# Performance work log

Measured on AMD Instinct MI355X. Metric: run time of the kernel, lower is better.

## Reference

```python
import jax, jax.numpy as jnp
import numpy as np

H = 2304; I_FF = 9216; NH = 8; NKV = 4; HD = 256; W = 4096; V = 65536
EPS = 1e-6; SOFTCAP = 30.0; HALF = HD // 2; POS = W // 2  # current decode position
WSCALE = 0.02


def rmsnorm(x, w, eps=EPS):
    return x * jax.lax.rsqrt(jnp.mean(x * x, axis=-1, keepdims=True) + eps) * w


def setup_inputs() -> dict:
    key = jax.random.key(0)
    ks = jax.random.split(key, 16)
    # RoPE angles for position POS
    inv_freq = 1.0 / (10000.0 ** (jnp.arange(HALF, dtype=jnp.float32) / HALF))
    ang = POS * inv_freq
    # attention mask: allow slots <= POS, block the rest
    slot = jnp.arange(W)
    mask = jnp.where(slot <= POS, 0.0, -1e9).astype(jnp.float32).reshape(1, 1, 1, W)
    # one-hot scatter selector for the cache write
    update_idx = jnp.zeros((1, 1, W, 1), jnp.float32).at[0, 0, POS, 0].set(1.0)
    return {
        "hidden_prev": jax.random.normal(ks[0], (1, 1, H), jnp.float32),
        "embed_token": jax.random.normal(ks[1], (1, 1, H), jnp.float32),
        "kv_k_in": jax.random.normal(ks[2], (1, NKV, W, HD), jnp.float32),
        "kv_v_in": jax.random.normal(ks[3], (1, NKV, W, HD), jnp.float32),
        "cos": jnp.cos(ang),
        "sin": jnp.sin(ang),
        "mask": mask,
        "update_idx": update_idx,
        "in_h_w": jax.random.normal(ks[4], (H, H), jnp.float32) * WSCALE,
        "in_e_w": jax.random.normal(ks[5], (H, H), jnp.float32) * WSCALE,
        "input_ln_w": jnp.ones((H,), jnp.float32),
        "post_attn_ln_w": jnp.ones((H,), jnp.float32),
        "pre_ffn_ln_w": jnp.ones((H,), jnp.float32),
        "post_ffn_ln_w": jnp.ones((H,), jnp.float32),
        "final_ln_w": jnp.ones((H,), jnp.float32),
        "q_w": jax.random.normal(ks[6], (NH * HD, H), jnp.float32) * WSCALE,
        "k_w": jax.random.normal(ks[7], (NKV * HD, H), jnp.float32) * WSCALE,
        "v_w": jax.random.normal(ks[8], (NKV * HD, H), jnp.float32) * WSCALE,
        "o_w": jax.random.normal(ks[9], (H, NH * HD), jnp.float32) * WSCALE,
        "q_norm_w": jnp.ones((HD,), jnp.float32),
        "k_norm_w": jnp.ones((HD,), jnp.float32),
        "gate_w": jax.random.normal(ks[10], (I_FF, H), jnp.float32) * WSCALE,
        "up_w": jax.random.normal(ks[11], (I_FF, H), jnp.float32) * WSCALE,
        "down_w": jax.random.normal(ks[12], (H, I_FF), jnp.float32) * WSCALE,
        "lm_head_w": jax.random.normal(ks[13], (V, H), jnp.float32) * WSCALE,
    }


def reference(hidden_prev, embed_token, kv_k_in, kv_v_in, cos, sin, mask, update_idx,
              in_h_w, in_e_w, input_ln_w, post_attn_ln_w, pre_ffn_ln_w, post_ffn_ln_w,
              final_ln_w, q_w, k_w, v_w, o_w, q_norm_w, k_norm_w, gate_w, up_w, down_w,
              lm_head_w):
    # dual input projection (1x1 convs == linear)
    x = hidden_prev @ in_h_w.T + embed_token @ in_e_w.T          # [1,1,H]
    residual = x
    hn = rmsnorm(x, input_ln_w)
    # QKV
    q = (hn @ q_w.T).reshape(1, NH, 1, HD)
    k = (hn @ k_w.T).reshape(1, NKV, 1, HD)
    v = (hn @ v_w.T).reshape(1, NKV, 1, HD)
    q = rmsnorm(q, q_norm_w)
    k = rmsnorm(k, k_norm_w)
    # RoPE (half-split rotation)
    cos_r = cos.reshape(1, 1, 1, HALF)
    sin_r = sin.reshape(1, 1, 1, HALF)
    q1, q2 = q[..., :HALF], q[..., HALF:]
    q = jnp.concatenate([q1 * cos_r - q2 * sin_r, q2 * cos_r + q1 * sin_r], axis=-1)
    k1, k2 = k[..., :HALF], k[..., HALF:]
    k_rot = jnp.concatenate([k1 * cos_r - k2 * sin_r, k2 * cos_r + k1 * sin_r], axis=-1)
    # multiply-based KV cache update
    keep = 1.0 - update_idx                                      # [1,1,W,1]
    kv_k_out = kv_k_in * keep + k_rot * update_idx               # [1,NKV,W,HD]
    kv_v_out = kv_v_in * keep + v * update_idx
    # GQA expansion
    n_rep = NH // NKV
    k_exp = jnp.repeat(kv_k_out, n_rep, axis=1)                  # [1,NH,W,HD]
    v_exp = jnp.repeat(kv_v_out, n_rep, axis=1)
    # fp32 attention
    scale = 1.0 / np.sqrt(HD)
    attn = jnp.einsum('bhqd,bhkd->bhqk', q, k_exp) * scale + mask
    p = jax.nn.softmax(attn, axis=-1)
    out = jnp.einsum('bhqk,bhkd->bhqd', p, v_exp).reshape(1, 1, NH * HD)
    h_attn = rmsnorm(out @ o_w.T, post_attn_ln_w)
    x = residual + h_attn
    residual = x
    # FFN (gelu-gated)
    hf = rmsnorm(x, pre_ffn_ln_w)
    d = (jax.nn.gelu(hf @ gate_w.T, approximate=False) * (hf @ up_w.T)) @ down_w.T
    x = residual + rmsnorm(d, post_ffn_ln_w)
    hidden_out = rmsnorm(x, final_ln_w)
    # lm_head + softcap + argmax
    logits = hidden_out @ lm_head_w.T                            # [1,1,V]
    logits = jnp.tanh(logits / SOFTCAP) * SOFTCAP
    idx = jnp.argmax(logits, axis=-1)                            # [1,1]
    top_k_indices = idx.reshape(1).astype(jnp.int32)
    top_k_values = jnp.take_along_axis(logits, idx[..., None], axis=-1).reshape(1)
    return (top_k_indices, top_k_values, hidden_out, kv_k_out, kv_v_out)
```

## Files before the change

### kernel.cpp

```cpp
#include <hip/hip_runtime.h>
#include <math.h>

#define H      2304
#define I_FF   9216
#define NH     8
#define NKV    4
#define HD     256
#define W_CTX  4096
#define V_SZ   65536
#define POS    2048
#define NCHUNK 32
#define CHUNK  64
#define NATTN  (NH * NCHUNK)
#define NBLK_ATTN_TOTAL 2048
#define EPS    1e-6f
#define NBLK_IN   576
#define NBLK_LM   4096

enum {
  WS_X    = 0,
  WS_SSQ  = 2304,
  WS_QKV  = 2880,
  WS_ML   = 6976,
  WS_YP   = 7488,
  WS_HRAW = 73024,
  WS_X2   = 75328,
  WS_ACT  = 77632,
  WS_DV   = 86848,
  WS_PART = 89152,
  WS_END  = 97344
};

typedef float f4v __attribute__((ext_vector_type(4)));
typedef float f2v __attribute__((ext_vector_type(2)));

__device__ __forceinline__ f4v ntload4(const float* p) {
  return __builtin_nontemporal_load((const f4v*)p);
}
__device__ __forceinline__ float wave_reduce_sum(float v) {
#pragma unroll
  for (int off = 32; off; off >>= 1) v += __shfl_down(v, off);
  return v;
}
__device__ __forceinline__ float wave_reduce_max(float v) {
#pragma unroll
  for (int off = 32; off; off >>= 1) v = fmaxf(v, __shfl_down(v, off));
  return v;
}
__device__ __forceinline__ float dot4(float4 a, float4 b) {
  return a.x * b.x + a.y * b.y + a.z * b.z + a.w * b.w;
}
__device__ __forceinline__ float dot4n(f4v a, float4 b) {
  return a.x * b.x + a.y * b.y + a.z * b.z + a.w * b.w;
}

__global__ void k_input(const float* __restrict__ Wh, const float* __restrict__ We,
                        const float* __restrict__ hprev, const float* __restrict__ emb,
                        float* __restrict__ x, float* __restrict__ ssq_part) {
  __shared__ float sv[4];
  int wv = threadIdx.x >> 6, lane = threadIdx.x & 63;
  int row = blockIdx.x * 4 + wv;
  const float* wh = Wh + (size_t)row * H;
  const float* we = We + (size_t)row * H;
  const float4* hp = (const float4*)hprev;
  const float4* em = (const float4*)emb;
  float acc = 0.f;
#pragma unroll
  for (int i = 0; i < H / 256; ++i) {
    int idx = lane + i * 64;
    acc += dot4n(ntload4(wh + idx * 4), hp[idx]);
    acc += dot4n(ntload4(we + idx * 4), em[idx]);
  }
  acc = wave_reduce_sum(acc);
  if (lane == 0) { x[row] = acc; sv[wv] = acc * acc; }
  __syncthreads();
  if (threadIdx.x == 0) ssq_part[blockIdx.x] = sv[0] + sv[1] + sv[2] + sv[3];
}

__global__ void k_qkv(const float* __restrict__ qw, const float* __restrict__ kw,
                      const float* __restrict__ vw, const float* __restrict__ x,
                      const float* __restrict__ lnw, const float* __restrict__ ssq,
                      float* __restrict__ qkv) {
  __shared__ float sred[4];
  int tid = threadIdx.x, lane = tid & 63, wv = tid >> 6;
  float s = ssq[tid] + ssq[tid + 256] + (tid < 64 ? ssq[tid + 512] : 0.f);
  s = wave_reduce_sum(s);
  if (lane == 0) sred[wv] = s;
  __syncthreads();
  float scale = rsqrtf((sred[0] + sred[1] + sred[2] + sred[3]) / (float)H + EPS);

  int row = (blockIdx.x * 256 + tid) >> 6;
  const float* Wrow;
  if (row < 2048)      Wrow = qw + (size_t)row * H;
  else if (row < 3072) Wrow = kw + (size_t)(row - 2048) * H;
  else                 Wrow = vw + (size_t)(row - 3072) * H;
  const float4* xv = (const float4*)x;
  const float4* l4 = (const float4*)lnw;
  float acc = 0.f;
#pragma unroll
  for (int i = 0; i < H / 256; ++i) {
    int idx = lane + i * 64;
    f4v w = ntload4(Wrow + idx * 4);
    float4 hx = xv[idx], wl = l4[idx];
    acc += w.x * (hx.x * scale * wl.x) + w.y * (hx.y * scale * wl.y) +
           w.z * (hx.z * scale * wl.z) + w.w * (hx.w * scale * wl.w);
  }
  acc = wave_reduce_sum(acc);
  if (lane == 0) qkv[row] = acc;
}

__global__ void k_attn(const float* __restrict__ qkv, const float* __restrict__ qnw,
                       const float* __restrict__ knw, const float* __restrict__ cosv,
                       const float* __restrict__ sinv, const float* __restrict__ kin,
                       const float* __restrict__ vin, float* __restrict__ kv_k_out,
                       float* __restrict__ kv_v_out, float* __restrict__ ml,
                       float* __restrict__ ypart,
                       const f2v* __restrict__ kin2, const f2v* __restrict__ vin2,
                       f2v* __restrict__ kout2, f2v* __restrict__ vout2) {
  int b = blockIdx.x;
  int tid = threadIdx.x, lane = tid & 63, wv = tid >> 6;
  if (b >= NATTN) {
    size_t cb = b - NATTN;
    const size_t n = (size_t)NKV * W_CTX * HD / 2;
    const size_t stride = (size_t)(NBLK_ATTN_TOTAL - NATTN) * 256;
    for (size_t i = cb * 256 + tid; i < n; i += stride) {
      int slot = (int)((i >> 7) & (W_CTX - 1));
      if (slot != POS) {
        __builtin_nontemporal_store(kin2[i], kout2 + i);
        __builtin_nontemporal_store(vin2[i], vout2 + i);
      }
    }
    return;
  }
  int h = b >> 5, j = b & 31, kvh = h >> 1;
  __shared__ float qs[HD], ks[HD], sc[CHUNK + 1];
  __shared__ float sredq[4], sredk[4];
  float qv = qkv[h * HD + tid];
  float kv = qkv[2048 + kvh * HD + tid];
  float pq = wave_reduce_sum(qv * qv);
  float pk = wave_reduce_sum(kv * kv);
  if (lane == 0) { sredq[wv] = pq; sredk[wv] = pk; }
  __syncthreads();
  float sq = rsqrtf((sredq[0] + sredq[1] + sredq[2] + sredq[3]) / (float)HD + EPS);
  float sk = rsqrtf((sredk[0] + sredk[1] + sredk[2] + sredk[3]) / (float)HD + EPS);
  qs[tid] = qv * sq * qnw[tid];
  ks[tid] = kv * sk * knw[tid];
  __syncthreads();
  if (tid < HD / 2) {
    float c = cosv[tid], s2 = sinv[tid];
    float q1 = qs[tid], q2 = qs[tid + 128];
    qs[tid] = q1 * c - q2 * s2;  qs[tid + 128] = q2 * c + q1 * s2;
    float k1 = ks[tid], k2 = ks[tid + 128];
    ks[tid] = k1 * c - k2 * s2;  ks[tid + 128] = k2 * c + k1 * s2;
  }
  __syncthreads();
  if (j == 0 && (h & 1) == 0) {
    kv_k_out[((size_t)kvh * W_CTX + POS) * HD + tid] = ks[tid];
    kv_v_out[((size_t)kvh * W_CTX + POS) * HD + tid] = qkv[3072 + kvh * HD + tid];
  }
  int base = j * CHUNK;
  int clen = (j == NCHUNK - 1) ? CHUNK + 1 : CHUNK;
  float4 qf = ((const float4*)qs)[lane];
  const float4* Kb = (const float4*)(kin + ((size_t)kvh * W_CTX + base) * HD);
  for (int i = wv; i < clen; i += 4) {
    float4 kk = (i < CHUNK) ? Kb[(size_t)i * (HD / 4) + lane] : ((const float4*)ks)[lane];
    float acc = dot4(qf, kk);
    acc = wave_reduce_sum(acc);
    if (lane == 0) sc[i] = acc * 0.0625f;
  }
  __syncthreads();
  float m = -1e30f;
  for (int i = tid; i < clen; i += 256) m = fmaxf(m, sc[i]);
  m = wave_reduce_max(m);
  if (lane == 0) sredq[wv] = m;
  __syncthreads();
  float M = fmaxf(fmaxf(sredq[0], sredq[1]), fmaxf(sredq[2], sredq[3]));
  float ssum = 0.f;
  for (int i = tid; i < clen; i += 256) { float e = expf(sc[i] - M); sc[i] = e; ssum += e; }
  ssum = wave_reduce_sum(ssum);
  if (lane == 0) sredk[wv] = ssum;
  __syncthreads();
  if (tid == 0) {
    ml[(h * NCHUNK + j) * 2]     = M;
    ml[(h * NCHUNK + j) * 2 + 1] = sredk[0] + sredk[1] + sredk[2] + sredk[3];
  }
  const float* Vb = vin + ((size_t)kvh * W_CTX + base) * HD;
  float a0 = 0.f, a1 = 0.f, a2 = 0.f, a3 = 0.f;
  for (int s = 0; s < CHUNK; s += 4) {
    a0 += sc[s]     * Vb[(size_t)s * HD + tid];
    a1 += sc[s + 1] * Vb[(size_t)(s + 1) * HD + tid];
    a2 += sc[s + 2] * Vb[(size_t)(s + 2) * HD + tid];
    a3 += sc[s + 3] * Vb[(size_t)(s + 3) * HD + tid];
  }
  if (clen > CHUNK) a0 += sc[CHUNK] * qkv[3072 + kvh * HD + tid];
  ypart[(size_t)(h * NCHUNK + j) * HD + tid] = a0 + a1 + a2 + a3;
}

__global__ void k_o(const float* __restrict__ ow, const float* __restrict__ ml,
                    const float* __restrict__ yp, float* __restrict__ hraw) {
  __shared__ float lmm[256], lml[256], ew[256], Lh[8];
  __shared__ float atts[NH * HD];
  int tid = threadIdx.x, lane = tid & 63, wv = tid >> 6;
  lmm[tid] = ml[2 * tid];
  lml[tid] = ml[2 * tid + 1];
  __syncthreads();
  int hh = tid >> 5;
  float M = -1e30f;
#pragma unroll 8
  for (int jj = 0; jj < 32; ++jj) M = fmaxf(M, lmm[hh * 32 + jj]);
  ew[tid] = expf(lmm[tid] - M);
  __syncthreads();
  if ((tid & 31) == 0) {
    float L = 0.f;
#pragma unroll 8
    for (int jj = 0; jj < 32; ++jj) L += lml[tid + jj] * ew[tid + jj];
    Lh[tid >> 5] = L;
  }
  __syncthreads();
  for (int h2 = 0; h2 < 8; ++h2) {
    float acc = 0.f;
#pragma unroll 8
    for (int jj = 0; jj < 32; ++jj)
      acc += ew[h2 * 32 + jj] * yp[(size_t)(h2 * 32 + jj) * HD + tid];
    atts[h2 * HD + tid] = acc / Lh[h2];
  }
  __syncthreads();
  int row = blockIdx.x * 4 + wv;
  const float* wr = ow + (size_t)row * (NH * HD);
  const float4* xv = (const float4*)atts;
  float acc = 0.f;
#pragma unroll
  for (int i = 0; i < (NH * HD) / 256; ++i) {
    int idx = lane + i * 64;
    acc += dot4n(ntload4(wr + idx * 4), xv[idx]);
  }
  acc = wave_reduce_sum(acc);
  if (lane == 0) hraw[row] = acc;
}

__global__ void k_gateup(const float* __restrict__ gw, const float* __restrict__ uw,
                         const float* __restrict__ x, const float* __restrict__ hraw,
                         const float* __restrict__ w_post, const float* __restrict__ w_pre,
                         float* __restrict__ x2_out, float* __restrict__ act) {
  __shared__ float hfs[H];
  __shared__ float srA[4], srB[4];
  int tid = threadIdx.x, lane = tid & 63, wv = tid >> 6;
  float lh[9], lx2[9];
  float ss = 0.f;
#pragma unroll
  for (int k = 0; k < 9; ++k) { lh[k] = hraw[tid + k * 256]; ss += lh[k] * lh[k]; }
  ss = wave_reduce_sum(ss);
  if (lane == 0) srA[wv] = ss;
  __syncthreads();
  float sc1 = rsqrtf((srA[0] + srA[1] + srA[2] + srA[3]) / (float)H + EPS);
  float ss2 = 0.f;
#pragma unroll
  for (int k = 0; k < 9; ++k) {
    int i = tid + k * 256;
    float v = x[i] + lh[k] * sc1 * w_post[i];
    lx2[k] = v; ss2 += v * v;
  }
  ss2 = wave_reduce_sum(ss2);
  if (lane == 0) srB[wv] = ss2;
  __syncthreads();
  float sc2 = rsqrtf((srB[0] + srB[1] + srB[2] + srB[3]) / (float)H + EPS);
#pragma unroll
  for (int k = 0; k < 9; ++k) { int i = tid + k * 256; hfs[i] = lx2[k] * sc2 * w_pre[i]; }
  if (blockIdx.x == 0) {
#pragma unroll
    for (int k = 0; k < 9; ++k) { int i = tid + k * 256; x2_out[i] = lx2[k]; }
  }
  __syncthreads();
  int row = (blockIdx.x * 256 + tid) >> 6;
  const float* g4 = gw + (size_t)row * H;
  const float* u4 = uw + (size_t)row * H;
  const float4* h4 = (const float4*)hfs;
  float ag = 0.f, au = 0.f;
#pragma unroll
  for (int i = 0; i < H / 256; ++i) {
    int idx = lane + i * 64;
    float4 hh2 = h4[idx];
    ag += dot4n(ntload4(g4 + idx * 4), hh2);
    au += dot4n(ntload4(u4 + idx * 4), hh2);
  }
  ag = wave_reduce_sum(ag);
  au = wave_reduce_sum(au);
  if (lane == 0) {
    float gl = 0.5f * ag * (1.f + erff(ag * 0.70710678118f));
    act[row] = gl * au;
  }
}

__global__ void k_down(const float* __restrict__ dw, const float* __restrict__ actv,
                       float* __restrict__ dv) {
  int row  = (blockIdx.x * 256 + threadIdx.x) >> 6;
  int lane = threadIdx.x & 63;
  const float* wr = dw + (size_t)row * I_FF;
  const float4* xv = (const float4*)actv;
  float acc = 0.f;
#pragma unroll 4
  for (int i = 0; i < I_FF / 256; ++i) {
    int idx = lane + i * 64;
    acc += dot4n(ntload4(wr + idx * 4), xv[idx]);
  }
  acc = wave_reduce_sum(acc);
  if (lane == 0) dv[row] = acc;
}

__global__ void k_lmhead(const float* __restrict__ Wm, const float* __restrict__ x2,
                         const float* __restrict__ dv, const float* __restrict__ w_post,
                         const float* __restrict__ w_fin, float* __restrict__ hid_out,
                         float2* __restrict__ partials) {
  __shared__ float hid[H];
  __shared__ float srA[4], srB[4];
  __shared__ float bv[4]; __shared__ int bi[4];
  int tid = threadIdx.x, lane = tid & 63, wv = tid >> 6;
  float ld[9], lx3[9];
  float ss = 0.f;
#pragma unroll
  for (int k = 0; k < 9; ++k) { ld[k] = dv[tid + k * 256]; ss += ld[k] * ld[k]; }
  ss = wave_reduce_sum(ss);
  if (lane == 0) srA[wv] = ss;
  __syncthreads();
  float sc1 = rsqrtf((srA[0] + srA[1] + srA[2] + srA[3]) / (float)H + EPS);
  float ss2 = 0.f;
#pragma unroll
  for (int k = 0; k < 9; ++k) {
    int i = tid + k * 256;
    float v = x2[i] + ld[k] * sc1 * w_post[i];
    lx3[k] = v; ss2 += v * v;
  }
  ss2 = wave_reduce_sum(ss2);
  if (lane == 0) srB[wv] = ss2;
  __syncthreads();
  float sc2 = rsqrtf((srB[0] + srB[1] + srB[2] + srB[3]) / (float)H + EPS);
#pragma unroll
  for (int k = 0; k < 9; ++k) { int i = tid + k * 256; hid[i] = lx3[k] * sc2 * w_fin[i]; }
  if (blockIdx.x == 0) {
#pragma unroll
    for (int k = 0; k < 9; ++k) { int i = tid + k * 256; hid_out[i] = hid[i]; }
  }
  __syncthreads();
  int gw   = (blockIdx.x * 256 + tid) >> 6;
  const float4* hv = (const float4*)hid;
  int row0 = gw * 4;
  const float* w0 = Wm + (size_t)(row0 + 0) * H;
  const float* w1 = Wm + (size_t)(row0 + 1) * H;
  const float* w2 = Wm + (size_t)(row0 + 2) * H;
  const float* w3 = Wm + (size_t)(row0 + 3) * H;
  float a0 = 0.f, a1 = 0.f, a2 = 0.f, a3 = 0.f;
#pragma unroll
  for (int i = 0; i < H / 256; ++i) {
    int idx = lane + i * 64;
    float4 b = hv[idx];
    a0 += dot4n(ntload4(w0 + idx * 4), b);
    a1 += dot4n(ntload4(w1 + idx * 4), b);
    a2 += dot4n(ntload4(w2 + idx * 4), b);
    a3 += dot4n(ntload4(w3 + idx * 4), b);
  }
  a0 = wave_reduce_sum(a0);
  a1 = wave_reduce_sum(a1);
  a2 = wave_reduce_sum(a2);
  a3 = wave_reduce_sum(a3);
  if (lane == 0) {
    float l0 = 30.f * tanhf(a0 * (1.f / 30.f));
    float l1 = 30.f * tanhf(a1 * (1.f / 30.f));
    float l2 = 30.f * tanhf(a2 * (1.f / 30.f));
    float l3 = 30.f * tanhf(a3 * (1.f / 30.f));
    float best = l0; int bidx = row0;
    if (l1 > best) { best = l1; bidx = row0 + 1; }
    if (l2 > best) { best = l2; bidx = row0 + 2; }
    if (l3 > best) { best = l3; bidx = row0 + 3; }
    bv[wv] = best; bi[wv] = bidx;
  }
  __syncthreads();
  if (tid == 0) {
    float B = bv[0]; int I = bi[0];
    for (int i = 1; i < 4; ++i)
      if (bv[i] > B || (bv[i] == B && bi[i] < I)) { B = bv[i]; I = bi[i]; }
    partials[blockIdx.x] = make_float2(B, (float)I);
  }
}

__global__ void k_argmax_final(const float2* __restrict__ partials, int n,
                               float* __restrict__ out) {
  __shared__ float bv[256]; __shared__ int bi[256];
  int tid = threadIdx.x;
  float best = -1e30f; int bidx = 0x7fffffff;
  for (int i = tid; i < n; i += 256) {
    float2 p = partials[i];
    int pi = (int)p.y;
    if (p.x > best || (p.x == best && pi < bidx)) { best = p.x; bidx = pi; }
  }
  bv[tid] = best; bi[tid] = bidx; __syncthreads();
  for (int s = 128; s; s >>= 1) {
    if (tid < s) {
      if (bv[tid + s] > bv[tid] || (bv[tid + s] == bv[tid] && bi[tid + s] < bi[tid])) {
        bv[tid] = bv[tid + s]; bi[tid] = bi[tid + s];
      }
    }
    __syncthreads();
  }
  if (tid == 0) { out[0] = (float)bi[0]; out[1] = bv[0]; }
}

extern "C" void kernel_launch(void* const* d_in, const int* in_sizes, int n_in,
                              void* d_out, int out_size, void* d_ws, size_t ws_size,
                              hipStream_t stream) {
  const float* hidden_prev = (const float*)d_in[0];
  const float* embed_token = (const float*)d_in[1];
  const float* kv_k_in     = (const float*)d_in[2];
  const float* kv_v_in     = (const float*)d_in[3];
  const float* cosv        = (const float*)d_in[4];
  const float* sinv        = (const float*)d_in[5];
  const float* in_h_w      = (const float*)d_in[8];
  const float* in_e_w      = (const float*)d_in[9];
  const float* input_ln_w  = (const float*)d_in[10];
  const float* post_attn_w = (const float*)d_in[11];
  const float* pre_ffn_w   = (const float*)d_in[12];
  const float* post_ffn_w  = (const float*)d_in[13];
  const float* final_ln_w  = (const float*)d_in[14];
  const float* q_w         = (const float*)d_in[15];
  const float* k_w         = (const float*)d_in[16];
  const float* v_w         = (const float*)d_in[17];
  const float* o_w         = (const float*)d_in[18];
  const float* q_norm_w    = (const float*)d_in[19];
  const float* k_norm_w    = (const float*)d_in[20];
  const float* gate_w      = (const float*)d_in[21];
  const float* up_w        = (const float*)d_in[22];
  const float* down_w      = (const float*)d_in[23];
  const float* lm_head_w   = (const float*)d_in[24];

  float* out     = (float*)d_out;
  float* out_hid = out + 2;
  float* out_kvk = out + 2 + H;
  float* out_kvv = out_kvk + (size_t)NKV * W_CTX * HD;
  float* ws      = (float*)d_ws;

  k_input<<<NBLK_IN, 256, 0, stream>>>(in_h_w, in_e_w, hidden_prev, embed_token,
                                       ws + WS_X, ws + WS_SSQ);
  k_qkv<<<1024, 256, 0, stream>>>(q_w, k_w, v_w, ws + WS_X, input_ln_w,
                                  ws + WS_SSQ, ws + WS_QKV);
  k_attn<<<NBLK_ATTN_TOTAL, 256, 0, stream>>>(
      ws + WS_QKV, q_norm_w, k_norm_w, cosv, sinv, kv_k_in, kv_v_in,
      out_kvk, out_kvv, ws + WS_ML, ws + WS_YP,
      (const f2v*)kv_k_in, (const f2v*)kv_v_in, (f2v*)out_kvk, (f2v*)out_kvv);
  k_o<<<H / 4, 256, 0, stream>>>(o_w, ws + WS_ML, ws + WS_YP, ws + WS_HRAW);
  k_gateup<<<I_FF / 4, 256, 0, stream>>>(gate_w, up_w, ws + WS_X, ws + WS_HRAW,
                                         post_attn_w, pre_ffn_w, ws + WS_X2, ws + WS_ACT);
  k_down<<<H / 4, 256, 0, stream>>>(down_w, ws + WS_ACT, ws + WS_DV);
  k_lmhead<<<NBLK_LM, 256, 0, stream>>>(lm_head_w, ws + WS_X2, ws + WS_DV,
                                        post_ffn_w, final_ln_w, out_hid,
                                        (float2*)(ws + WS_PART));
  k_argmax_final<<<1, 256, 0, stream>>>((const float2*)(ws + WS_PART), NBLK_LM, out);

  (void)in_sizes; (void)n_in; (void)out_size; (void)ws_size;
}
```

Baseline: 205.1 us.

## Prefetch first weight chunk before prologue reductions; two rows per wave in gateup

In k_qkv, k_gateup and k_lmhead, each wave now issues its first weight load before the block-wide RMSnorm prologue and barriers, so the memory latency overlaps the reduction work. k_gateup now computes two gate/up rows per wave and launches half as many blocks, which halves how often the per-block norm prologue is recomputed. The attention combine in k_o is restructured so each wave handles two heads with float4 loads instead of every thread looping over all eight heads with scalar loads. The extra in-flight registers could reduce occupancy, and the halved gateup grid lowers parallelism.

```diff
diff --git a/kernel.cpp b/kernel.cpp
--- a/kernel.cpp
+++ b/kernel.cpp
@@ -83,22 +83,25 @@
                       float* __restrict__ qkv) {
   __shared__ float sred[4];
   int tid = threadIdx.x, lane = tid & 63, wv = tid >> 6;
-  float s = ssq[tid] + ssq[tid + 256] + (tid < 64 ? ssq[tid + 512] : 0.f);
-  s = wave_reduce_sum(s);
-  if (lane == 0) sred[wv] = s;
-  __syncthreads();
-  float scale = rsqrtf((sred[0] + sred[1] + sred[2] + sred[3]) / (float)H + EPS);
-
   int row = (blockIdx.x * 256 + tid) >> 6;
   const float* Wrow;
   if (row < 2048)      Wrow = qw + (size_t)row * H;
   else if (row < 3072) Wrow = kw + (size_t)(row - 2048) * H;
   else                 Wrow = vw + (size_t)(row - 3072) * H;
+  f4v p0 = ntload4(Wrow + lane * 4);
+  float s = ssq[tid] + ssq[tid + 256] + (tid < 64 ? ssq[tid + 512] : 0.f);
+  s = wave_reduce_sum(s);
+  if (lane == 0) sred[wv] = s;
+  __syncthreads();
+  float scale = rsqrtf((sred[0] + sred[1] + sred[2] + sred[3]) / (float)H + EPS);
+
   const float4* xv = (const float4*)x;
   const float4* l4 = (const float4*)lnw;
-  float acc = 0.f;
-#pragma unroll
-  for (int i = 0; i < H / 256; ++i) {
+  float4 hx0 = xv[lane], wl0 = l4[lane];
+  float acc = p0.x * (hx0.x * scale * wl0.x) + p0.y * (hx0.y * scale * wl0.y) +
+              p0.z * (hx0.z * scale * wl0.z) + p0.w * (hx0.w * scale * wl0.w);
+#pragma unroll
+  for (int i = 1; i < H / 256; ++i) {
     int idx = lane + i * 64;
     f4v w = ntload4(Wrow + idx * 4);
     float4 hx = xv[idx], wl = l4[idx];
@@ -217,12 +220,20 @@
     Lh[tid >> 5] = L;
   }
   __syncthreads();
-  for (int h2 = 0; h2 < 8; ++h2) {
-    float acc = 0.f;
+#pragma unroll
+  for (int ho = 0; ho < 2; ++ho) {
+    int h2 = 2 * wv + ho;
+    float4 acc = make_float4(0.f, 0.f, 0.f, 0.f);
 #pragma unroll 8
-    for (int jj = 0; jj < 32; ++jj)
-      acc += ew[h2 * 32 + jj] * yp[(size_t)(h2 * 32 + jj) * HD + tid];
-    atts[h2 * HD + tid] = acc / Lh[h2];
+    for (int jj = 0; jj < 32; ++jj) {
+      const float4* yr = (const float4*)(yp + (size_t)(h2 * 32 + jj) * HD);
+      float4 v = yr[lane];
+      float w = ew[h2 * 32 + jj];
+      acc.x += w * v.x; acc.y += w * v.y; acc.z += w * v.z; acc.w += w * v.w;
+    }
+    float invL = 1.f / Lh[h2];
+    float4 r = make_float4(acc.x * invL, acc.y * invL, acc.z * invL, acc.w * invL);
+    ((float4*)atts)[h2 * (HD / 4) + lane] = r;
   }
   __syncthreads();
   int row = blockIdx.x * 4 + wv;
@@ -245,6 +256,13 @@
   __shared__ float hfs[H];
   __shared__ float srA[4], srB[4];
   int tid = threadIdx.x, lane = tid & 63, wv = tid >> 6;
+  int r0 = (blockIdx.x * 4 + wv) * 2;
+  const float* g0 = gw + (size_t)r0 * H;
+  const float* g1 = gw + (size_t)(r0 + 1) * H;
+  const float* u0 = uw + (size_t)r0 * H;
+  const float* u1 = uw + (size_t)(r0 + 1) * H;
+  f4v pg0 = ntload4(g0 + lane * 4), pg1 = ntload4(g1 + lane * 4);
+  f4v pu0 = ntload4(u0 + lane * 4), pu1 = ntload4(u1 + lane * 4);
   float lh[9], lx2[9];
   float ss = 0.f;
 #pragma unroll
@@ -271,23 +289,28 @@
     for (int k = 0; k < 9; ++k) { int i = tid + k * 256; x2_out[i] = lx2[k]; }
   }
   __syncthreads();
-  int row = (blockIdx.x * 256 + tid) >> 6;
-  const float* g4 = gw + (size_t)row * H;
-  const float* u4 = uw + (size_t)row * H;
   const float4* h4 = (const float4*)hfs;
-  float ag = 0.f, au = 0.f;
-#pragma unroll
-  for (int i = 0; i < H / 256; ++i) {
-    int idx = lane + i * 64;
-    float4 hh2 = h4[idx];
-    ag += dot4n(ntload4(g4 + idx * 4), hh2);
-    au += dot4n(ntload4(u4 + idx * 4), hh2);
-  }
-  ag = wave_reduce_sum(ag);
-  au = wave_reduce_sum(au);
+  float4 hh0 = h4[lane];
+  float ag0 = dot4n(pg0, hh0), ag1 = dot4n(pg1, hh0);
+  float au0 = dot4n(pu0, hh0), au1 = dot4n(pu1, hh0);
+#pragma unroll
+  for (int i = 1; i < H / 256; ++i) {
+    int idx = lane + i * 64;
+    float4 hh = h4[idx];
+    ag0 += dot4n(ntload4(g0 + idx * 4), hh);
+    ag1 += dot4n(ntload4(g1 + idx * 4), hh);
+    au0 += dot4n(ntload4(u0 + idx * 4), hh);
+    au1 += dot4n(ntload4(u1 + idx * 4), hh);
+  }
+  ag0 = wave_reduce_sum(ag0);
+  ag1 = wave_reduce_sum(ag1);
+  au0 = wave_reduce_sum(au0);
+  au1 = wave_reduce_sum(au1);
   if (lane == 0) {
-    float gl = 0.5f * ag * (1.f + erff(ag * 0.70710678118f));
-    act[row] = gl * au;
+    float gl0 = 0.5f * ag0 * (1.f + erff(ag0 * 0.70710678118f));
+    float gl1 = 0.5f * ag1 * (1.f + erff(ag1 * 0.70710678118f));
+    act[r0]     = gl0 * au0;
+    act[r0 + 1] = gl1 * au1;
   }
 }
 
@@ -315,42 +338,46 @@
   __shared__ float srA[4], srB[4];
   __shared__ float bv[4]; __shared__ int bi[4];
   int tid = threadIdx.x, lane = tid & 63, wv = tid >> 6;
-  float ld[9], lx3[9];
-  float ss = 0.f;
-#pragma unroll
-  for (int k = 0; k < 9; ++k) { ld[k] = dv[tid + k * 256]; ss += ld[k] * ld[k]; }
-  ss = wave_reduce_sum(ss);
-  if (lane == 0) srA[wv] = ss;
-  __syncthreads();
-  float sc1 = rsqrtf((srA[0] + srA[1] + srA[2] + srA[3]) / (float)H + EPS);
-  float ss2 = 0.f;
-#pragma unroll
-  for (int k = 0; k < 9; ++k) {
-    int i = tid + k * 256;
-    float v = x2[i] + ld[k] * sc1 * w_post[i];
-    lx3[k] = v; ss2 += v * v;
-  }
-  ss2 = wave_reduce_sum(ss2);
-  if (lane == 0) srB[wv] = ss2;
-  __syncthreads();
-  float sc2 = rsqrtf((srB[0] + srB[1] + srB[2] + srB[3]) / (float)H + EPS);
-#pragma unroll
-  for (int k = 0; k < 9; ++k) { int i = tid + k * 256; hid[i] = lx3[k] * sc2 * w_fin[i]; }
-  if (blockIdx.x == 0) {
-#pragma unroll
-    for (int k = 0; k < 9; ++k) { int i = tid + k * 256; hid_out[i] = hid[i]; }
-  }
-  __syncthreads();
   int gw   = (blockIdx.x * 256 + tid) >> 6;
-  const float4* hv = (const float4*)hid;
   int row0 = gw * 4;
   const float* w0 = Wm + (size_t)(row0 + 0) * H;
   const float* w1 = Wm + (size_t)(row0 + 1) * H;
   const float* w2 = Wm + (size_t)(row0 + 2) * H;
   const float* w3 = Wm + (size_t)(row0 + 3) * H;
-  float a0 = 0.f, a1 = 0.f, a2 = 0.f, a3 = 0.f;
-#pragma unroll
-  for (int i = 0; i < H / 256; ++i) {
+  f4v p0 = ntload4(w0 + lane * 4), p1 = ntload4(w1 + lane * 4);
+  f4v p2 = ntload4(w2 + lane * 4), p3 = ntload4(w3 + lane * 4);
+  float ld[9], lx3[9];
+  float ss = 0.f;
+#pragma unroll
+  for (int k = 0; k < 9; ++k) { ld[k] = dv[tid + k * 256]; ss += ld[k] * ld[k]; }
+  ss = wave_reduce_sum(ss);
+  if (lane == 0) srA[wv] = ss;
+  __syncthreads();
+  float sc1 = rsqrtf((srA[0] + srA[1] + srA[2] + srA[3]) / (float)H + EPS);
+  float ss2 = 0.f;
+#pragma unroll
+  for (int k = 0; k < 9; ++k) {
+    int i = tid + k * 256;
+    float v = x2[i] + ld[k] * sc1 * w_post[i];
+    lx3[k] = v; ss2 += v * v;
+  }
+  ss2 = wave_reduce_sum(ss2);
+  if (lane == 0) srB[wv] = ss2;
+  __syncthreads();
+  float sc2 = rsqrtf((srB[0] + srB[1] + srB[2] + srB[3]) / (float)H + EPS);
+#pragma unroll
+  for (int k = 0; k < 9; ++k) { int i = tid + k * 256; hid[i] = lx3[k] * sc2 * w_fin[i]; }
+  if (blockIdx.x == 0) {
+#pragma unroll
+    for (int k = 0; k < 9; ++k) { int i = tid + k * 256; hid_out[i] = hid[i]; }
+  }
+  __syncthreads();
+  const float4* hv = (const float4*)hid;
+  float4 b0 = hv[lane];
+  float a0 = dot4n(p0, b0), a1 = dot4n(p1, b0);
+  float a2 = dot4n(p2, b0), a3 = dot4n(p3, b0);
+#pragma unroll
+  for (int i = 1; i < H / 256; ++i) {
     int idx = lane + i * 64;
     float4 b = hv[idx];
     a0 += dot4n(ntload4(w0 + idx * 4), b);
@@ -446,7 +473,7 @@
       out_kvk, out_kvv, ws + WS_ML, ws + WS_YP,
       (const f2v*)kv_k_in, (const f2v*)kv_v_in, (f2v*)out_kvk, (f2v*)out_kvv);
   k_o<<<H / 4, 256, 0, stream>>>(o_w, ws + WS_ML, ws + WS_YP, ws + WS_HRAW);
-  k_gateup<<<I_FF / 4, 256, 0, stream>>>(gate_w, up_w, ws + WS_X, ws + WS_HRAW,
+  k_gateup<<<I_FF / 8, 256, 0, stream>>>(gate_w, up_w, ws + WS_X, ws + WS_HRAW,
                                          post_attn_w, pre_ffn_w, ws + WS_X2, ws + WS_ACT);
   k_down<<<H / 4, 256, 0, stream>>>(down_w, ws + WS_ACT, ws + WS_DV);
   k_lmhead<<<NBLK_LM, 256, 0, stream>>>(lm_head_w, ws + WS_X2, ws + WS_DV,
```

Result: faster. 196.2 us (-4.3%).
